# Performance work log

Measured on AMD Instinct MI355X. Metric: run time of the kernel, lower is better.

## Reference

```python
import jax, jax.numpy as jnp
import numpy as np

# SemiConv2d with semifield_type='MaxMin':
#   out[n,oc,i,j] = max_{ic,kh,kw} min(x_pad[n,ic,i+kh,j+kw], kernel[oc,ic,kh,kw])
# stride=1, 'same' padding with -inf (identity of max).

def setup_inputs() -> dict:
    key = jax.random.key(0)
    kx, kk = jax.random.split(key)
    x = jax.random.normal(kx, (8, 32, 96, 96), dtype=jnp.float32)
    kernel = jax.random.normal(kk, (32, 32, 3, 3), dtype=jnp.float32)
    return {"x": x, "kernel": kernel}


def reference(x, kernel):
    N, IC, H, W = x.shape
    OC, IC2, KH, KW = kernel.shape
    assert IC == IC2
    # same padding for k=3, stride=1 (left=top=1, right=bottom=1)
    p = KH - 1
    top = left = p // 2
    bot = right = p - top
    xp = jnp.pad(x, ((0, 0), (0, 0), (top, bot), (left, right)),
                 constant_values=-jnp.inf)
    out = None
    # small fixed loop over kernel taps (KH*KW = 9); vectorized over N, OC, IC, H, W
    for kh in range(KH):
        for kw in range(KW):
            win = xp[:, :, kh:kh + H, kw:kw + W]           # [N, IC, H, W]
            k_tap = kernel[:, :, kh, kw]                   # [OC, IC]
            # min over values, max over input channels -> [N, OC, H, W]
            v = jnp.max(jnp.minimum(win[:, None], k_tap[None, :, :, None, None]), axis=2)
            out = v if out is None else jnp.maximum(out, v)
    return out
```

## Files before the change

### kernel.cpp

```cpp
#include <hip/hip_runtime.h>
#include <math.h>
#include <stdint.h>


#define HH 96
#define WW 96
#define CIN 32
#define OCN 32
#define XQ_ROWS 98
#define XQ_W 48
#define XQ_SLICE (XQ_ROWS * XQ_W)
#define XQ_TOTAL (256 * XQ_SLICE)
#define K2_TOTAL (16 * 32 * 2 * 9)
#define WS_NEED ((size_t)XQ_TOTAL * 8 + (size_t)K2_TOTAL * 4)
#define NEGH2 0xFC00FC00u

typedef _Float16 h2 __attribute__((ext_vector_type(2)));

__device__ __forceinline__ uint32_t pkmin_vs(uint32_t x, uint32_t k) {
    uint32_t d;
    asm("v_pk_min_f16 %0, %1, %2" : "=v"(d) : "v"(x), "s"(k));
    return d;
}
__device__ __forceinline__ uint32_t pkmax(uint32_t a, uint32_t b) {
    uint32_t d;
    asm("v_pk_max_f16 %0, %1, %2" : "=v"(d) : "v"(a), "v"(b));
    return d;
}
__device__ __forceinline__ uint32_t packh2(float lo, float hi) {
    h2 p = {(_Float16)lo, (_Float16)hi};
    return __builtin_bit_cast(uint32_t, p);
}

__global__ __launch_bounds__(256) void setup_xq(const float* __restrict__ x,
                                                uint2* __restrict__ xq) {
    int idx = blockIdx.x * 256 + threadIdx.x;
    int j  = idx % XQ_W;
    int t  = idx / XQ_W;
    int hp = t % XQ_ROWS;
    int s  = t / XQ_ROWS;
    int h  = hp - 1;
    bool hv = (h >= 0) && (h < HH);
    const float* row = x + ((size_t)s * HH + (hv ? h : 0)) * WW;
    float a = (hv && j > 0)        ? row[2 * j - 1] : -INFINITY;
    float b = hv                   ? row[2 * j]     : -INFINITY;
    float c = hv                   ? row[2 * j + 1] : -INFINITY;
    float d = (hv && j < XQ_W - 1) ? row[2 * j + 2] : -INFINITY;
    uint2 v;
    v.x = packh2(a, b);
    v.y = packh2(c, d);
    xq[idx] = v;
}

__global__ __launch_bounds__(256) void setup_k(const float* __restrict__ kk,
                                               uint32_t* __restrict__ k2) {
    int idx = blockIdx.x * 256 + threadIdx.x;
    int tap = idx % 9;
    int oc2 = (idx / 9) % 2;
    int ic  = (idx / 18) % CIN;
    int ocb = idx / (18 * CIN);
    float v = kk[(((ocb * 2 + oc2) * CIN) + ic) * 9 + tap];
    k2[idx] = packh2(v, v);
}

__global__ __launch_bounds__(192, 8) void semiconv_f16(const uint2* __restrict__ xq,
                                                       const uint32_t* __restrict__ k2,
                                                       float* __restrict__ out) {
    const int tid = threadIdx.x;
    const int jj = tid % 48;
    const int hr = tid / 48;
    const int b  = blockIdx.x;
    const int hp  = b % 24;
    const int t   = b / 24;
    const int ocb = t & 15;
    const int n   = t >> 4;
    const int h   = hp * 4 + hr;

    const uint2* xp = xq + ((size_t)(n * CIN) * XQ_ROWS + h) * XQ_W + jj;
    const uint32_t* kp = k2 + (size_t)ocb * CIN * 18;

    uint32_t acc[2] = {NEGH2, NEGH2};

    for (int ic0 = 0; ic0 < CIN; ic0 += 2) {
        uint2 q[2][3];
#pragma unroll
        for (int u = 0; u < 2; ++u)
#pragma unroll
            for (int r = 0; r < 3; ++r)
                q[u][r] = xp[(size_t)u * XQ_SLICE + r * XQ_W];

#pragma unroll
        for (int u = 0; u < 2; ++u) {
            uint32_t tap[9];
#pragma unroll
            for (int r = 0; r < 3; ++r) {
                tap[r * 3 + 0] = q[u][r].x;
                tap[r * 3 + 1] = __builtin_amdgcn_alignbit(q[u][r].y, q[u][r].x, 16);
                tap[r * 3 + 2] = q[u][r].y;
            }
            const uint32_t* kq0 = kp + (ic0 + u) * 18;
#pragma unroll
            for (int oc = 0; oc < 2; ++oc) {
                const uint32_t* kq = kq0 + oc * 9;
                uint32_t m0 = pkmin_vs(tap[0], kq[0]);
                uint32_t m1 = pkmin_vs(tap[1], kq[1]);
                uint32_t m2 = pkmin_vs(tap[2], kq[2]);
                uint32_t m3 = pkmin_vs(tap[3], kq[3]);
                uint32_t m4 = pkmin_vs(tap[4], kq[4]);
                uint32_t m5 = pkmin_vs(tap[5], kq[5]);
                uint32_t m6 = pkmin_vs(tap[6], kq[6]);
                uint32_t m7 = pkmin_vs(tap[7], kq[7]);
                uint32_t m8 = pkmin_vs(tap[8], kq[8]);
                uint32_t t01 = pkmax(m0, m1), t23 = pkmax(m2, m3);
                uint32_t t45 = pkmax(m4, m5), t67 = pkmax(m6, m7);
                uint32_t tt  = pkmax(pkmax(t01, t23), pkmax(t45, t67));
                acc[oc] = pkmax(acc[oc], pkmax(tt, m8));
            }
        }
        xp += 2 * XQ_SLICE;
    }

#pragma unroll
    for (int oc = 0; oc < 2; ++oc) {
        h2 a = __builtin_bit_cast(h2, acc[oc]);
        float2 v = make_float2((float)a.x, (float)a.y);
        *(float2*)(out + (((size_t)(n * OCN + ocb * 2 + oc)) * HH + h) * WW + 2 * jj) = v;
    }
}

#define NEGINF (-INFINITY)
__global__ __launch_bounds__(192, 8) void semiconv2d_f32(
    const float* __restrict__ x, const float* __restrict__ kk, float* __restrict__ out)
{
    const int tid = threadIdx.x;
    const int w  = tid % WW;
    const int hr = tid / WW;
    const int b   = blockIdx.x;
    const int ocb = b & 7;
    const int hp  = (b >> 3) % 48;
    const int n   = (b >> 3) / 48;
    const int h   = hp * 2 + hr;
    const int oc0 = ocb * 4;
    float a0[4], a1[4], a2[4];
#pragma unroll
    for (int i = 0; i < 4; ++i) { a0[i] = NEGINF; a1[i] = NEGINF; a2[i] = NEGINF; }
    const bool vm = (h > 0), vp = (h < HH - 1);
    const int hm  = vm ? h - 1 : h;
    const int hpl = vp ? h + 1 : h;
    const int cm  = (w > 0) ? -1 : 0;
    const int cp  = (w < WW - 1) ? 1 : 0;
    const float* rm = x + ((size_t)(n * CIN) * HH + hm)  * WW + w;
    const float* r1 = x + ((size_t)(n * CIN) * HH + h)   * WW + w;
    const float* rp = x + ((size_t)(n * CIN) * HH + hpl) * WW + w;
#pragma unroll 2
    for (int ic = 0; ic < CIN; ++ic) {
        float r00 = vm ? rm[cm] : NEGINF, r01 = vm ? rm[0] : NEGINF, r02 = vm ? rm[cp] : NEGINF;
        float r10 = r1[cm], r11 = r1[0], r12 = r1[cp];
        float r20 = vp ? rp[cm] : NEGINF, r21 = vp ? rp[0] : NEGINF, r22 = vp ? rp[cp] : NEGINF;
#pragma unroll
        for (int oc = 0; oc < 4; ++oc) {
            const float* kq = kk + (size_t)(((oc0 + oc) * CIN + ic)) * 9;
            a0[oc] = fmaxf(fmaxf(a0[oc], fminf(r00, kq[0])), fmaxf(fminf(r10, kq[3]), fminf(r20, kq[6])));
            a1[oc] = fmaxf(fmaxf(a1[oc], fminf(r01, kq[1])), fmaxf(fminf(r11, kq[4]), fminf(r21, kq[7])));
            a2[oc] = fmaxf(fmaxf(a2[oc], fminf(r02, kq[2])), fmaxf(fminf(r12, kq[5]), fminf(r22, kq[8])));
        }
        rm += HH * WW; r1 += HH * WW; rp += HH * WW;
    }
#pragma unroll
    for (int oc = 0; oc < 4; ++oc) {
        float v0 = (w > 0)      ? a0[oc] : NEGINF;
        float v2 = (w < WW - 1) ? a2[oc] : NEGINF;
        out[(((size_t)(n * OCN + oc0 + oc)) * HH + h) * WW + w] = fmaxf(fmaxf(v0, a1[oc]), v2);
    }
}

extern "C" void kernel_launch(void* const* d_in, const int* in_sizes, int n_in,
                              void* d_out, int out_size, void* d_ws, size_t ws_size,
                              hipStream_t stream) {
    const float* x  = (const float*)d_in[0];
    const float* kk = (const float*)d_in[1];
    float* out      = (float*)d_out;
    if (ws_size >= WS_NEED) {
        uint2* xq    = (uint2*)d_ws;
        uint32_t* k2 = (uint32_t*)(xq + XQ_TOTAL);
        setup_xq<<<dim3(XQ_TOTAL / 256), dim3(256), 0, stream>>>(x, xq);
        setup_k<<<dim3(K2_TOTAL / 256), dim3(256), 0, stream>>>(kk, k2);
        semiconv_f16<<<dim3(8 * 16 * 24), dim3(192), 0, stream>>>(xq, k2, out);
    } else {
        semiconv2d_f32<<<dim3(8 * 48 * 8), dim3(192), 0, stream>>>(x, kk, out);
    }
}
```

Baseline: 101.9 us.

## Sort kernel taps by weight descending and exit early per output channel

A setup kernel sorts each output channel's 288 (ic,tap) weights in descending order into a table that holds each packed weight, its input offset and its shift. The main kernel handles one output channel per block, walks the sorted taps four at a time and stops once every lane's accumulator is at least the next weight, since later min(x,k) terms cannot raise the max. This aims to skip most of the min/max work and the loads that go with it, at the cost of gathered loads from per-tap offsets, a vote at each step, and half as many outputs per thread as before.

```diff
diff --git a/kernel.cpp b/kernel.cpp
--- a/kernel.cpp
+++ b/kernel.cpp
@@ -11,15 +11,21 @@
 #define XQ_W 48
 #define XQ_SLICE (XQ_ROWS * XQ_W)
 #define XQ_TOTAL (256 * XQ_SLICE)
-#define K2_TOTAL (16 * 32 * 2 * 9)
-#define WS_NEED ((size_t)XQ_TOTAL * 8 + (size_t)K2_TOTAL * 4)
+#define TB_TOTAL (32 * 288)
+#define WS_NEED ((size_t)XQ_TOTAL * 8 + (size_t)TB_TOTAL * 16)
 #define NEGH2 0xFC00FC00u
 
 typedef _Float16 h2 __attribute__((ext_vector_type(2)));
+typedef uint32_t u2a4 __attribute__((ext_vector_type(2), aligned(4)));
 
 __device__ __forceinline__ uint32_t pkmin_vs(uint32_t x, uint32_t k) {
     uint32_t d;
     asm("v_pk_min_f16 %0, %1, %2" : "=v"(d) : "v"(x), "s"(k));
+    return d;
+}
+__device__ __forceinline__ uint32_t pkmin_vv(uint32_t a, uint32_t b) {
+    uint32_t d;
+    asm("v_pk_min_f16 %0, %1, %2" : "=v"(d) : "v"(a), "v"(b));
     return d;
 }
 __device__ __forceinline__ uint32_t pkmax(uint32_t a, uint32_t b) {
@@ -52,80 +58,75 @@
     xq[idx] = v;
 }
 
-__global__ __launch_bounds__(256) void setup_k(const float* __restrict__ kk,
-                                               uint32_t* __restrict__ k2) {
-    int idx = blockIdx.x * 256 + threadIdx.x;
-    int tap = idx % 9;
-    int oc2 = (idx / 9) % 2;
-    int ic  = (idx / 18) % CIN;
-    int ocb = idx / (18 * CIN);
-    float v = kk[(((ocb * 2 + oc2) * CIN) + ic) * 9 + tap];
-    k2[idx] = packh2(v, v);
+__global__ void setup_tap(const float* __restrict__ kk, uint4* __restrict__ tbl) {
+    __shared__ float ks[288];
+    const int oc = blockIdx.x;
+    const int t  = threadIdx.x;
+    float k = kk[oc * 288 + t];
+    ks[t] = k;
+    __syncthreads();
+    int rank = 0;
+    for (int s = 0; s < 288; ++s) {
+        float kv = ks[s];
+        rank += (kv > k) || (kv == k && s < t);
+    }
+    const int ic = t / 9, tap = t % 9, dh = tap / 3, dw = tap % 3;
+    uint32_t off = (uint32_t)(ic * XQ_ROWS + dh) * (XQ_W * 8) + (dw == 2 ? 4u : 0u);
+    uint32_t sh  = (dw == 1) ? 16u : 0u;
+    tbl[oc * 288 + rank] = make_uint4(packh2(k, k), off, sh, 0u);
 }
 
-__global__ __launch_bounds__(192, 8) void semiconv_f16(const uint2* __restrict__ xq,
-                                                       const uint32_t* __restrict__ k2,
-                                                       float* __restrict__ out) {
+__device__ __forceinline__ uint32_t tapval(const char* xb, int vbyte, uint4 e) {
+    u2a4 q = *(const u2a4*)(xb + e.y + (uint32_t)vbyte);
+    uint32_t v = __builtin_amdgcn_alignbit(q.y, q.x, e.z);
+    return pkmin_vs(v, e.x);
+}
+
+__global__ __launch_bounds__(192, 8) void semiconv_ee(const char* __restrict__ xqb,
+                                                      const uint4* __restrict__ tbl,
+                                                      float* __restrict__ out) {
     const int tid = threadIdx.x;
     const int jj = tid % 48;
     const int hr = tid / 48;
     const int b  = blockIdx.x;
-    const int hp  = b % 24;
-    const int t   = b / 24;
-    const int ocb = t & 15;
-    const int n   = t >> 4;
-    const int h   = hp * 4 + hr;
+    const int hp = b % 24;
+    const int t  = b / 24;
+    const int oc = t & 31;
+    const int n  = t >> 5;
+    const int h  = hp * 4 + hr;
 
-    const uint2* xp = xq + ((size_t)(n * CIN) * XQ_ROWS + h) * XQ_W + jj;
-    const uint32_t* kp = k2 + (size_t)ocb * CIN * 18;
+    const char* xb = xqb + (size_t)n * CIN * XQ_SLICE * 8;
+    const int vbyte = (h * XQ_W + jj) * 8;
+    const uint4* tb = tbl + oc * 288;
 
-    uint32_t acc[2] = {NEGH2, NEGH2};
+    uint32_t acc = NEGH2;
+    uint4 e0 = tb[0], e1 = tb[1], e2 = tb[2], e3 = tb[3];
 
-    for (int ic0 = 0; ic0 < CIN; ic0 += 2) {
-        uint2 q[2][3];
-#pragma unroll
-        for (int u = 0; u < 2; ++u)
-#pragma unroll
-            for (int r = 0; r < 3; ++r)
-                q[u][r] = xp[(size_t)u * XQ_SLICE + r * XQ_W];
+    for (int c = 0; c < 72; ++c) {
+        uint4 f0, f1, f2, f3;
+        if (c < 71) {
+            const uint4* nb = tb + 4 * (c + 1);
+            f0 = nb[0]; f1 = nb[1]; f2 = nb[2]; f3 = nb[3];
+        }
+        uint32_t m0 = tapval(xb, vbyte, e0);
+        uint32_t m1 = tapval(xb, vbyte, e1);
+        uint32_t m2 = tapval(xb, vbyte, e2);
+        uint32_t m3 = tapval(xb, vbyte, e3);
+        acc = pkmax(acc, pkmax(pkmax(m0, m1), pkmax(m2, m3)));
 
-#pragma unroll
-        for (int u = 0; u < 2; ++u) {
-            uint32_t tap[9];
-#pragma unroll
-            for (int r = 0; r < 3; ++r) {
-                tap[r * 3 + 0] = q[u][r].x;
-                tap[r * 3 + 1] = __builtin_amdgcn_alignbit(q[u][r].y, q[u][r].x, 16);
-                tap[r * 3 + 2] = q[u][r].y;
-            }
-            const uint32_t* kq0 = kp + (ic0 + u) * 18;
-#pragma unroll
-            for (int oc = 0; oc < 2; ++oc) {
-                const uint32_t* kq = kq0 + oc * 9;
-                uint32_t m0 = pkmin_vs(tap[0], kq[0]);
-                uint32_t m1 = pkmin_vs(tap[1], kq[1]);
-                uint32_t m2 = pkmin_vs(tap[2], kq[2]);
-                uint32_t m3 = pkmin_vs(tap[3], kq[3]);
-                uint32_t m4 = pkmin_vs(tap[4], kq[4]);
-                uint32_t m5 = pkmin_vs(tap[5], kq[5]);
-                uint32_t m6 = pkmin_vs(tap[6], kq[6]);
-                uint32_t m7 = pkmin_vs(tap[7], kq[7]);
-                uint32_t m8 = pkmin_vs(tap[8], kq[8]);
-                uint32_t t01 = pkmax(m0, m1), t23 = pkmax(m2, m3);
-                uint32_t t45 = pkmax(m4, m5), t67 = pkmax(m6, m7);
-                uint32_t tt  = pkmax(pkmax(t01, t23), pkmax(t45, t67));
-                acc[oc] = pkmax(acc[oc], pkmax(tt, m8));
-            }
+        if (c < 71) {
+            uint32_t sw = __builtin_amdgcn_alignbit(acc, acc, 16);
+            uint32_t mn = pkmin_vv(acc, sw);
+            h2 a  = __builtin_bit_cast(h2, mn);
+            h2 kn = __builtin_bit_cast(h2, f0.x);
+            if (__all((float)a.x >= (float)kn.x)) break;
+            e0 = f0; e1 = f1; e2 = f2; e3 = f3;
         }
-        xp += 2 * XQ_SLICE;
     }
 
-#pragma unroll
-    for (int oc = 0; oc < 2; ++oc) {
-        h2 a = __builtin_bit_cast(h2, acc[oc]);
-        float2 v = make_float2((float)a.x, (float)a.y);
-        *(float2*)(out + (((size_t)(n * OCN + ocb * 2 + oc)) * HH + h) * WW + 2 * jj) = v;
-    }
+    h2 a = __builtin_bit_cast(h2, acc);
+    float2 v = make_float2((float)a.x, (float)a.y);
+    *(float2*)(out + (((size_t)(n * OCN + oc)) * HH + h) * WW + 2 * jj) = v;
 }
 
 #define NEGINF (-INFINITY)
@@ -181,11 +182,12 @@
     const float* kk = (const float*)d_in[1];
     float* out      = (float*)d_out;
     if (ws_size >= WS_NEED) {
-        uint2* xq    = (uint2*)d_ws;
-        uint32_t* k2 = (uint32_t*)(xq + XQ_TOTAL);
+        uint2* xq  = (uint2*)d_ws;
+        uint4* tbl = (uint4*)((char*)d_ws + (size_t)XQ_TOTAL * 8);
         setup_xq<<<dim3(XQ_TOTAL / 256), dim3(256), 0, stream>>>(x, xq);
-        setup_k<<<dim3(K2_TOTAL / 256), dim3(256), 0, stream>>>(kk, k2);
-        semiconv_f16<<<dim3(8 * 16 * 24), dim3(192), 0, stream>>>(xq, k2, out);
+        setup_tap<<<dim3(32), dim3(288), 0, stream>>>(kk, tbl);
+        semiconv_ee<<<dim3(8 * 32 * 24), dim3(192), 0, stream>>>(
+            (const char*)xq, tbl, out);
     } else {
         semiconv2d_f32<<<dim3(8 * 48 * 8), dim3(192), 0, stream>>>(x, kk, out);
     }
```

Result: no change. 101.6 us (-0.4%).

## Sort input channels by kernel max and exit early once accumulators dominate

Applied to the files above, without the earlier changes.

A new setup kernel ranks the input channels of each output-channel pair by their largest kernel value, from high to low. The main kernel then visits channels in that order. From the fifth channel pair on, it checks after each pair whether every accumulator in the wave is already at least the next channel's kernel maximum, and stops if so. The skip is exact because min(x,k) can never exceed k. It costs an extra small launch, table loads, a per-iteration wave-wide vote, and gathered channel addressing, and any saving depends on the data letting whole waves exit early.

```diff
diff --git a/kernel.cpp b/kernel.cpp
--- a/kernel.cpp
+++ b/kernel.cpp
@@ -12,7 +12,8 @@
 #define XQ_SLICE (XQ_ROWS * XQ_W)
 #define XQ_TOTAL (256 * XQ_SLICE)
 #define K2_TOTAL (16 * 32 * 2 * 9)
-#define WS_NEED ((size_t)XQ_TOTAL * 8 + (size_t)K2_TOTAL * 4)
+#define TB_TOTAL (16 * 32)
+#define WS_NEED ((size_t)XQ_TOTAL * 8 + (size_t)K2_TOTAL * 4 + (size_t)TB_TOTAL * 8)
 #define NEGH2 0xFC00FC00u
 
 typedef _Float16 h2 __attribute__((ext_vector_type(2)));
@@ -20,6 +21,11 @@
 __device__ __forceinline__ uint32_t pkmin_vs(uint32_t x, uint32_t k) {
     uint32_t d;
     asm("v_pk_min_f16 %0, %1, %2" : "=v"(d) : "v"(x), "s"(k));
+    return d;
+}
+__device__ __forceinline__ uint32_t pkmin_vv(uint32_t a, uint32_t b) {
+    uint32_t d;
+    asm("v_pk_min_f16 %0, %1, %2" : "=v"(d) : "v"(a), "v"(b));
     return d;
 }
 __device__ __forceinline__ uint32_t pkmax(uint32_t a, uint32_t b) {
@@ -63,9 +69,28 @@
     k2[idx] = packh2(v, v);
 }
 
-__global__ __launch_bounds__(192, 8) void semiconv_f16(const uint2* __restrict__ xq,
-                                                       const uint32_t* __restrict__ k2,
-                                                       float* __restrict__ out) {
+__global__ void setup_tbl(const float* __restrict__ kk, uint2* __restrict__ tbl) {
+    __shared__ float ms[32];
+    const int ocb = blockIdx.x;
+    const int ic  = threadIdx.x;
+    float m = -INFINITY;
+    for (int oc = 0; oc < 2; ++oc)
+        for (int t = 0; t < 9; ++t)
+            m = fmaxf(m, kk[(((ocb * 2 + oc) * CIN) + ic) * 9 + t]);
+    ms[ic] = m;
+    __syncthreads();
+    int rank = 0;
+    for (int s = 0; s < 32; ++s) {
+        float v = ms[s];
+        rank += (v > m) || (v == m && s < ic);
+    }
+    tbl[ocb * 32 + rank] = make_uint2(packh2(m, m), (uint32_t)ic);
+}
+
+__global__ __launch_bounds__(192, 8) void semiconv_ic_ee(const uint2* __restrict__ xq,
+                                                         const uint32_t* __restrict__ k2,
+                                                         const uint2* __restrict__ tbl,
+                                                         float* __restrict__ out) {
     const int tid = threadIdx.x;
     const int jj = tid % 48;
     const int hr = tid / 48;
@@ -76,18 +101,22 @@
     const int n   = t >> 4;
     const int h   = hp * 4 + hr;
 
-    const uint2* xp = xq + ((size_t)(n * CIN) * XQ_ROWS + h) * XQ_W + jj;
+    const uint2* xb = xq + (size_t)(n * CIN) * XQ_SLICE + h * XQ_W + jj;
     const uint32_t* kp = k2 + (size_t)ocb * CIN * 18;
+    const uint2* tb = tbl + ocb * 32;
 
     uint32_t acc[2] = {NEGH2, NEGH2};
 
-    for (int ic0 = 0; ic0 < CIN; ic0 += 2) {
+    for (int cc = 0; cc < 16; ++cc) {
+        uint2 e0 = tb[2 * cc], e1 = tb[2 * cc + 1];
+        const uint32_t ic0 = e0.y, ic1 = e1.y;
+
         uint2 q[2][3];
 #pragma unroll
-        for (int u = 0; u < 2; ++u)
-#pragma unroll
-            for (int r = 0; r < 3; ++r)
-                q[u][r] = xp[(size_t)u * XQ_SLICE + r * XQ_W];
+        for (int r = 0; r < 3; ++r) {
+            q[0][r] = xb[(size_t)ic0 * XQ_SLICE + r * XQ_W];
+            q[1][r] = xb[(size_t)ic1 * XQ_SLICE + r * XQ_W];
+        }
 
 #pragma unroll
         for (int u = 0; u < 2; ++u) {
@@ -98,7 +127,7 @@
                 tap[r * 3 + 1] = __builtin_amdgcn_alignbit(q[u][r].y, q[u][r].x, 16);
                 tap[r * 3 + 2] = q[u][r].y;
             }
-            const uint32_t* kq0 = kp + (ic0 + u) * 18;
+            const uint32_t* kq0 = kp + (u ? ic1 : ic0) * 18;
 #pragma unroll
             for (int oc = 0; oc < 2; ++oc) {
                 const uint32_t* kq = kq0 + oc * 9;
@@ -117,7 +146,15 @@
                 acc[oc] = pkmax(acc[oc], pkmax(tt, m8));
             }
         }
-        xp += 2 * XQ_SLICE;
+
+        if (cc >= 4 && cc < 15) {
+            uint32_t kn = tb[2 * (cc + 1)].x;
+            uint32_t mn = pkmin_vv(acc[0], acc[1]);
+            mn = pkmin_vv(mn, __builtin_amdgcn_alignbit(mn, mn, 16));
+            h2 A  = __builtin_bit_cast(h2, mn);
+            h2 KN = __builtin_bit_cast(h2, kn);
+            if (__all((float)A.x >= (float)KN.x)) break;
+        }
     }
 
 #pragma unroll
@@ -182,10 +219,12 @@
     float* out      = (float*)d_out;
     if (ws_size >= WS_NEED) {
         uint2* xq    = (uint2*)d_ws;
-        uint32_t* k2 = (uint32_t*)(xq + XQ_TOTAL);
+        uint32_t* k2 = (uint32_t*)((char*)d_ws + (size_t)XQ_TOTAL * 8);
+        uint2* tbl   = (uint2*)((char*)d_ws + (size_t)XQ_TOTAL * 8 + (size_t)K2_TOTAL * 4);
         setup_xq<<<dim3(XQ_TOTAL / 256), dim3(256), 0, stream>>>(x, xq);
         setup_k<<<dim3(K2_TOTAL / 256), dim3(256), 0, stream>>>(kk, k2);
-        semiconv_f16<<<dim3(8 * 16 * 24), dim3(192), 0, stream>>>(xq, k2, out);
+        setup_tbl<<<dim3(16), dim3(32), 0, stream>>>(kk, tbl);
+        semiconv_ic_ee<<<dim3(8 * 16 * 24), dim3(192), 0, stream>>>(xq, k2, tbl, out);
     } else {
         semiconv2d_f32<<<dim3(8 * 48 * 8), dim3(192), 0, stream>>>(x, kk, out);
     }
```

After: 104.5 us. +2.5%, slower.
